# Optimization experiments

Hardware: AMD Instinct MI355X
Metric: run time of the kernel (lower is better)

The kernel has to match this reference:

```python
import jax, jax.numpy as jnp
import numpy as np
from jax import lax

EPS = 1e-7   # keras.backend.epsilon()
NEG = -1e30  # log-space -inf surrogate


def setup_inputs() -> dict:
    key = jax.random.key(0)
    k1, k2 = jax.random.split(key)
    B, T, C, L = 512, 1024, 256, 64
    logits = jax.random.uniform(k1, (B, T, C), dtype=jnp.float32)
    y_pred = logits / jnp.sum(logits, axis=-1, keepdims=True)  # valid probability rows
    y_true = jax.random.randint(k2, (B, L), 0, C - 1, dtype=jnp.int32)  # avoid blank=C-1
    return {"y_true": y_true, "y_pred": y_pred}


def _ctc_loss(y_pred, y_true):
    # y_pred: [B,T,C] probabilities; y_true: [B,L] labels; blank = C-1,
    # input_length = T and label_length = L for all batch elements (as in the module).
    B, T, C = y_pred.shape
    L = y_true.shape[1]
    S = 2 * L + 1
    blank = C - 1
    lp = jnp.log(y_pred + EPS)  # [B,T,C]

    # extended label sequence: blank, l1, blank, l2, ..., blank  -> [B,S]
    ext = jnp.full((B, S), blank, dtype=jnp.int32).at[:, 1::2].set(y_true.astype(jnp.int32))
    # per-step emission log-probs gathered on the extended sequence: [T,B,S]
    lp_ext = jnp.take_along_axis(lp, ext[:, None, :], axis=2).transpose(1, 0, 2)

    # skip transition (s-2 -> s) allowed iff ext[s] != blank and ext[s] != ext[s-2]
    ext_sm2 = jnp.pad(ext, ((0, 0), (2, 0)), constant_values=blank)[:, :S]
    allow_skip = (ext != blank) & (ext != ext_sm2)  # [B,S]

    alpha0 = jnp.full((B, S), NEG, dtype=lp.dtype)
    alpha0 = alpha0.at[:, 0].set(lp_ext[0, :, 0]).at[:, 1].set(lp_ext[0, :, 1])

    def step(alpha, lp_t):
        a1 = alpha
        a2 = jnp.pad(alpha, ((0, 0), (1, 0)), constant_values=NEG)[:, :S]
        a3 = jnp.where(allow_skip,
                       jnp.pad(alpha, ((0, 0), (2, 0)), constant_values=NEG)[:, :S],
                       NEG)
        m = jnp.maximum(jnp.maximum(a1, a2), a3)
        new = m + jnp.log(jnp.exp(a1 - m) + jnp.exp(a2 - m) + jnp.exp(a3 - m)) + lp_t
        return new, None

    alpha, _ = lax.scan(step, alpha0, lp_ext[1:])
    # sequence ends on final blank or final label
    total = jnp.logaddexp(alpha[:, S - 1], alpha[:, S - 2])
    return -total[:, None]  # [B,1], matching expand_dims in ctc_batch_cost


def reference(y_true, y_pred):
    return _ctc_loss(y_pred, y_true)
```

## Files before the change

### kernel.cpp

```cpp
#include <hip/hip_runtime.h>
#include <stdint.h>


#define EPS 1e-7f
#define NEG -1e30f

constexpr int Bb = 512;
constexpr int Tt = 1024;
constexpr int Cc = 256;
constexpr int Ll = 64;
constexpr int BLANK = Cc - 1;
constexpr int D = 32;

#define WAITVM31() asm volatile("s_waitcnt vmcnt(31)" ::: "memory")

__device__ __forceinline__ void dma_row(const float* __restrict__ g,
                                        float* l) {
    __builtin_amdgcn_global_load_lds(
        (const __attribute__((address_space(1))) void*)g,
        (__attribute__((address_space(3))) void*)l, 16, 0, 0);
}

__global__ __launch_bounds__(64) void ctc_fwd_kernel(
    const int* __restrict__ y_true,
    const float* __restrict__ y_pred,
    float* __restrict__ out)
{
    const int b = blockIdx.x;
    const int lane = threadIdx.x;

    const float* __restrict__ row0 = y_pred + (size_t)b * Tt * Cc;

    __shared__ float ring[D * Cc];

    const int lab = y_true[b * Ll + lane];
    const int lab_prev = __shfl_up(lab, 1);
    const bool allow = (lane == 0) ? true : (lab != lab_prev);

    for (int t0 = 0; t0 < D; ++t0)
        dma_row(row0 + t0 * Cc + lane * 4, &ring[t0 * Cc]);

    WAITVM31();
    const float pl0 = ring[lab];
    const float pb0 = ring[BLANK];
    float ae = (lane == 0) ? __logf(pb0 + EPS) : NEG;
    float ao = (lane == 0) ? __logf(pl0 + EPS) : NEG;
    float a128 = NEG;

    dma_row(row0 + D * Cc + lane * 4, &ring[0]);
    WAITVM31();
    float glA = ring[1 * Cc + lab];
    float gbA = ring[1 * Cc + BLANK];
    dma_row(row0 + (D + 1) * Cc + lane * 4, &ring[1 * Cc]);
    WAITVM31();
    float glB = ring[2 * Cc + lab];
    float gbB = ring[2 * Cc + BLANK];

    auto update = [&](float gl, float gb) {
        const float lpl = __logf(gl + EPS);
        const float lpb = __logf(gb + EPS);
        float ao_up = __shfl_up(ao, 1);
        if (lane == 0) ao_up = NEG;

        const float m2 = fmaxf(ae, ao_up);
        const float ne =
            m2 + __logf(__expf(ae - m2) + __expf(ao_up - m2)) + lpb;

        const float a3 = allow ? ao_up : NEG;
        const float m3 = fmaxf(fmaxf(ao, ae), a3);
        const float no =
            m3 +
            __logf(__expf(ao - m3) + __expf(ae - m3) + __expf(a3 - m3)) +
            lpl;

        const float m1 = fmaxf(a128, ao);
        const float n128 =
            m1 + __logf(__expf(a128 - m1) + __expf(ao - m1)) + lpb;

        ae = ne;
        ao = no;
        a128 = n128;
    };

    for (int t = 1; t <= Tt - 3; t += 2) {
        update(glA, gbA);
        {
            const int tn = min(t + 1 + D, Tt - 1);
            dma_row(row0 + tn * Cc + lane * 4,
                    &ring[((t + 1) & (D - 1)) * Cc]);
            WAITVM31();
            const int s = (t + 2) & (D - 1);
            glA = ring[s * Cc + lab];
            gbA = ring[s * Cc + BLANK];
        }
        update(glB, gbB);
        {
            const int tn = min(t + 2 + D, Tt - 1);
            dma_row(row0 + tn * Cc + lane * 4,
                    &ring[((t + 2) & (D - 1)) * Cc]);
            WAITVM31();
            const int s = (t + 3) & (D - 1);
            glB = ring[s * Cc + lab];
            gbB = ring[s * Cc + BLANK];
        }
    }
    update(glA, gbA);

    if (lane == 63) {
        const float m = fmaxf(a128, ao);
        out[b] = -(m + __logf(__expf(a128 - m) + __expf(ao - m)));
    }
}

extern "C" void kernel_launch(void* const* d_in, const int* in_sizes, int n_in,
                              void* d_out, int out_size, void* d_ws,
                              size_t ws_size, hipStream_t stream) {
    const int* y_true = (const int*)d_in[0];
    const float* y_pred = (const float*)d_in[1];
    float* out = (float*)d_out;

    ctc_fwd_kernel<<<dim3(Bb), dim3(64), 0, stream>>>(y_true, y_pred, out);
}
```

Measured before the change: 799.2 us.

## Replace per-row LDS ring with chunked double-buffered DMA prefetch

Replaces the per-timestep DMA plus waitcnt ring buffer with two 32-row chunks loaded into LDS by global_load_lds, with one wait per chunk. Each 32-step inner loop is fully unrolled so the LDS reads can be scheduled ahead of the serial recurrence. The goal is to take the memory wait off every step of the dependency chain and keep more loads in flight. In exchange, LDS use per block doubles to 64KB, which may limit how many blocks share a CU.

Result: no change. 809.0 us (+1.2%).

```diff
diff --git a/kernel.cpp b/kernel.cpp
--- a/kernel.cpp
+++ b/kernel.cpp
@@ -10,9 +10,8 @@
 constexpr int Cc = 256;
 constexpr int Ll = 64;
 constexpr int BLANK = Cc - 1;
-constexpr int D = 32;
-
-#define WAITVM31() asm volatile("s_waitcnt vmcnt(31)" ::: "memory")
+constexpr int CH = 32;
+constexpr int NCH = Tt / CH;
 
 __device__ __forceinline__ void dma_row(const float* __restrict__ g,
                                         float* l) {
@@ -21,7 +20,7 @@
         (__attribute__((address_space(3))) void*)l, 16, 0, 0);
 }
 
-__global__ __launch_bounds__(64) void ctc_fwd_kernel(
+__global__ __launch_bounds__(64, 1) void ctc_fwd_kernel(
     const int* __restrict__ y_true,
     const float* __restrict__ y_pred,
     float* __restrict__ out)
@@ -31,30 +30,27 @@
 
     const float* __restrict__ row0 = y_pred + (size_t)b * Tt * Cc;
 
-    __shared__ float ring[D * Cc];
+    __shared__ float ring[2 * CH * Cc];
 
     const int lab = y_true[b * Ll + lane];
     const int lab_prev = __shfl_up(lab, 1);
     const bool allow = (lane == 0) ? true : (lab != lab_prev);
 
-    for (int t0 = 0; t0 < D; ++t0)
-        dma_row(row0 + t0 * Cc + lane * 4, &ring[t0 * Cc]);
+    for (int r = 0; r < CH; ++r)
+        dma_row(row0 + r * Cc + lane * 4, &ring[r * Cc]);
+    for (int r = 0; r < CH; ++r)
+        dma_row(row0 + (CH + r) * Cc + lane * 4, &ring[(CH + r) * Cc]);
 
-    WAITVM31();
-    const float pl0 = ring[lab];
-    const float pb0 = ring[BLANK];
-    float ae = (lane == 0) ? __logf(pb0 + EPS) : NEG;
-    float ao = (lane == 0) ? __logf(pl0 + EPS) : NEG;
-    float a128 = NEG;
+    asm volatile("s_waitcnt vmcnt(32)" ::: "memory");
 
-    dma_row(row0 + D * Cc + lane * 4, &ring[0]);
-    WAITVM31();
-    float glA = ring[1 * Cc + lab];
-    float gbA = ring[1 * Cc + BLANK];
-    dma_row(row0 + (D + 1) * Cc + lane * 4, &ring[1 * Cc]);
-    WAITVM31();
-    float glB = ring[2 * Cc + lab];
-    float gbB = ring[2 * Cc + BLANK];
+    float ae, ao, a128;
+    {
+        const float pl0 = ring[lab];
+        const float pb0 = ring[BLANK];
+        ae = (lane == 0) ? __logf(pb0 + EPS) : NEG;
+        ao = (lane == 0) ? __logf(pl0 + EPS) : NEG;
+        a128 = NEG;
+    }
 
     auto update = [&](float gl, float gb) {
         const float lpl = __logf(gl + EPS);
@@ -82,29 +78,25 @@
         a128 = n128;
     };
 
-    for (int t = 1; t <= Tt - 3; t += 2) {
-        update(glA, gbA);
-        {
-            const int tn = min(t + 1 + D, Tt - 1);
-            dma_row(row0 + tn * Cc + lane * 4,
-                    &ring[((t + 1) & (D - 1)) * Cc]);
-            WAITVM31();
-            const int s = (t + 2) & (D - 1);
-            glA = ring[s * Cc + lab];
-            gbA = ring[s * Cc + BLANK];
+#pragma unroll
+    for (int r = 1; r < CH; ++r)
+        update(ring[r * Cc + lab], ring[r * Cc + BLANK]);
+
+    for (int c = 1; c < NCH; ++c) {
+        const float* buf = &ring[(c & 1) * CH * Cc];
+        float* nbuf = &ring[((c + 1) & 1) * CH * Cc];
+        if (c + 1 < NCH) {
+            const float* src = row0 + (size_t)(c + 1) * CH * Cc;
+            for (int r = 0; r < CH; ++r)
+                dma_row(src + r * Cc + lane * 4, nbuf + r * Cc);
+            asm volatile("s_waitcnt vmcnt(32)" ::: "memory");
+        } else {
+            asm volatile("s_waitcnt vmcnt(0)" ::: "memory");
         }
-        update(glB, gbB);
-        {
-            const int tn = min(t + 2 + D, Tt - 1);
-            dma_row(row0 + tn * Cc + lane * 4,
-                    &ring[((t + 2) & (D - 1)) * Cc]);
-            WAITVM31();
-            const int s = (t + 3) & (D - 1);
-            glB = ring[s * Cc + lab];
-            gbB = ring[s * Cc + BLANK];
-        }
+#pragma unroll
+        for (int r = 0; r < CH; ++r)
+            update(buf[r * Cc + lab], buf[r * Cc + BLANK]);
     }
-    update(glA, gbA);
 
     if (lane == 63) {
         const float m = fmaxf(a128, ao);
```
